# Performance work log

Hardware: AMD Instinct MI355X
Metric: run time of the kernel (lower is better)

## Reference

```python
import jax, jax.numpy as jnp
import numpy as np

B, S, D = 4, 512, 2048      # batch, seq, hidden
DFF = 5632                   # SwiGLU intermediate
E, TOPK, R = 8, 2, 16        # experts, top-k, lora rank
SCALE = 32.0 / 16.0          # lora alpha / r


def setup_inputs() -> dict:
    key = jax.random.key(0)
    ks = jax.random.split(key, 18)
    rn = lambda k, shape, s=0.02: (jax.random.normal(k, shape, dtype=jnp.float32) * s)
    return {
        "data": jax.random.normal(ks[0], (B, S, D), dtype=jnp.float32),
        # shared base SwiGLU MLP (gate/up/down projections)
        "W1": rn(ks[1], (DFF, D)),
        "W3": rn(ks[2], (DFF, D)),
        "W2": rn(ks[3], (D, DFF)),
        # MixLoRA MoE adapter: router gate + per-expert LoRA on w1/w3/w2
        "gate_W": rn(ks[4], (E, D)),
        "A1": rn(ks[5], (E, R, D)), "B1": rn(ks[6], (E, DFF, R)),
        "A3": rn(ks[7], (E, R, D)), "B3": rn(ks[8], (E, DFF, R)),
        "A2": rn(ks[9], (E, R, DFF)), "B2": rn(ks[10], (E, D, R)),
        # plain LoRA adapter (second batch segment, _lora_forward path)
        "la1": rn(ks[11], (R, D)), "lb1": rn(ks[12], (DFF, R)),
        "la3": rn(ks[13], (R, D)), "lb3": rn(ks[14], (DFF, R)),
        "la2": rn(ks[15], (R, DFF)), "lb2": rn(ks[16], (D, R)),
    }


def reference(data, W1, W3, W2, gate_W, A1, B1, A3, B3, A2, B2,
              la1, lb1, la3, lb3, la2, lb2):
    half = B // 2

    # ---- segment 0: MixLoRA MoE adapter ----
    x = data[:half].reshape(-1, D)                      # [N, D] tokens
    N = x.shape[0]
    logits = x @ gate_W.T                               # [N, E] router logits
    probs = jax.nn.softmax(logits, axis=-1)
    topw, topi = jax.lax.top_k(probs, TOPK)
    topw = topw / jnp.sum(topw, axis=-1, keepdims=True)
    # dense routing weights (zero for non-selected experts)
    wd = jnp.zeros((N, E), x.dtype).at[jnp.arange(N)[:, None], topi].set(topw)

    bg = x @ W1.T                                       # [N, DFF] base gate proj
    bu = x @ W3.T                                       # [N, DFF] base up proj
    dg = jnp.einsum('enr,efr->enf', jnp.einsum('nd,erd->enr', x, A1), B1)
    du = jnp.einsum('enr,efr->enf', jnp.einsum('nd,erd->enr', x, A3), B3)
    h = jax.nn.silu(bg[None] + SCALE * dg) * (bu[None] + SCALE * du)  # [E,N,DFF]
    oe = jnp.einsum('enf,df->end', h, W2) \
        + SCALE * jnp.einsum('enr,edr->end', jnp.einsum('enf,erf->enr', h, A2), B2)
    moe_out = jnp.einsum('ne,end->nd', wd, oe).reshape(half, S, D)

    # ---- segment 1: plain LoRA adapter (_lora_forward) ----
    x2 = data[half:]                                    # [half, S, D]
    g2 = jax.nn.silu(x2 @ W1.T + SCALE * ((x2 @ la1.T) @ lb1.T))
    u2 = x2 @ W3.T + SCALE * ((x2 @ la3.T) @ lb3.T)
    h2 = g2 * u2
    out2 = h2 @ W2.T + SCALE * ((h2 @ la2.T) @ lb2.T)

    # index_copy over contiguous per-segment ranges == concat along dim 0
    final = jnp.concatenate([moe_out, out2], axis=0)    # [B, S, D]
    return final, logits
```

## Files before the change

### kernel.cpp

```cpp
#include <hip/hip_runtime.h>
#include <hip/hip_bf16.h>

#define DEVI __device__ __forceinline__

typedef __attribute__((ext_vector_type(8))) short short8;
typedef __attribute__((ext_vector_type(4))) float f32x4;

constexpr int D    = 2048;
constexpr int DFF  = 5632;
constexpr int NTOK = 2048;
constexpr int NMOE = 1024;
constexpr float KSCALE = 2.0f;

constexpr int NW      = 11776;
constexpr int COL_A1  = 11264;
constexpr int COL_A3  = 11392;
constexpr int COL_LA1 = 11520;
constexpr int COL_LA3 = 11536;

DEVI float bf2f(unsigned short u) { return __uint_as_float(((unsigned)u) << 16); }
DEVI unsigned short f2bf(float f) {
  unsigned u = __float_as_uint(f);
  u += 0x7FFFu + ((u >> 16) & 1u);
  return (unsigned short)(u >> 16);
}
DEVI float silu(float x) { return x / (1.f + __expf(-x)); }

struct CastSegs {
  const float* src[14];
  unsigned short* dst[14];
  int blk_end[14];
};

__global__ __launch_bounds__(256) void cast_segs_kernel(CastSegs cs) {
  int b = blockIdx.x;
  int s = 0;
  #pragma unroll
  for (int i = 0; i < 14; ++i) if (b >= cs.blk_end[i]) s = i + 1;
  int bstart = (s == 0) ? 0 : cs.blk_end[s - 1];
  size_t idx = ((size_t)(b - bstart) * 256 + threadIdx.x) * 4;
  float4 v = *(const float4*)(cs.src[s] + idx);
  ushort4 o;
  o.x = f2bf(v.x); o.y = f2bf(v.y); o.z = f2bf(v.z); o.w = f2bf(v.w);
  *(ushort4*)(cs.dst[s] + idx) = o;
}

__global__ __launch_bounds__(256) void transpose_ra_kernel(const float* __restrict__ A2,
                                                           const float* __restrict__ la2,
                                                           unsigned short* __restrict__ A2tb,
                                                           unsigned short* __restrict__ la2tb) {
  int f = blockIdx.x * 256 + threadIdx.x;
  int e = blockIdx.y;
  const float* src = (e < 8) ? (A2 + (size_t)e * 16 * DFF) : la2;
  unsigned short* dst = (e < 8) ? (A2tb + (size_t)e * DFF * 16) : la2tb;
  unsigned short tmp[16];
  #pragma unroll
  for (int r = 0; r < 16; ++r) tmp[r] = f2bf(src[(size_t)r * DFF + f]);
  #pragma unroll
  for (int r = 0; r < 16; ++r) dst[(size_t)f * 16 + r] = tmp[r];
}

__global__ __launch_bounds__(256) void gate_kernel(const float* __restrict__ x,
                                                   const float* __restrict__ gW,
                                                   float* __restrict__ logits_out,
                                                   int* __restrict__ gidx,
                                                   float* __restrict__ gwt) {
  int t = blockIdx.x * 4 + (threadIdx.x >> 6);
  int lane = threadIdx.x & 63;
  const float* xr = x + (size_t)t * D;
  float acc[8];
  #pragma unroll
  for (int e = 0; e < 8; ++e) acc[e] = 0.f;
  for (int k = lane; k < D; k += 64) {
    float xv = xr[k];
    #pragma unroll
    for (int e = 0; e < 8; ++e) acc[e] = fmaf(xv, gW[e * D + k], acc[e]);
  }
  #pragma unroll
  for (int e = 0; e < 8; ++e) {
    float v = acc[e];
    #pragma unroll
    for (int s = 32; s > 0; s >>= 1) v += __shfl_xor(v, s);
    acc[e] = v;
  }
  if (lane == 0) {
    #pragma unroll
    for (int e = 0; e < 8; ++e) logits_out[(size_t)t * 8 + e] = acc[e];
    int i1 = 0;
    #pragma unroll
    for (int e = 1; e < 8; ++e) if (acc[e] > acc[i1]) i1 = e;
    int i2 = (i1 == 0) ? 1 : 0;
    #pragma unroll
    for (int e = 0; e < 8; ++e) if (e != i1 && acc[e] > acc[i2]) i2 = e;
    float w1 = 1.f / (1.f + expf(acc[i2] - acc[i1]));
    gidx[t * 2] = i1; gidx[t * 2 + 1] = i2;
    gwt[t * 2] = w1;  gwt[t * 2 + 1] = 1.f - w1;
  }
}

typedef const void __attribute__((address_space(1)))* gp1_t;
typedef void __attribute__((address_space(3)))* lp3_t;
DEVI void gload_lds16(const void* g, void* l) {
  __builtin_amdgcn_global_load_lds((gp1_t)g, (lp3_t)l, 16, 0, 0);
}
#define S_BARRIER() asm volatile("s_barrier" ::: "memory")
#define LGKM0() do { asm volatile("s_waitcnt lgkmcnt(0)" ::: "memory"); \
                     __builtin_amdgcn_sched_barrier(0); } while (0)

template <int N> DEVI void vmcnt_() {
  static_assert(N == 0 || N == 4 || N == 8, "enumerate literals");
  if constexpr (N == 0)  asm volatile("s_waitcnt vmcnt(0)" ::: "memory");
  if constexpr (N == 4)  asm volatile("s_waitcnt vmcnt(4)" ::: "memory");
  if constexpr (N == 8)  asm volatile("s_waitcnt vmcnt(8)" ::: "memory");
}

template <int BM, int BN, int WM, int WN, int MINW, int EPI>
__global__ __launch_bounds__(WM * WN * 64, MINW) void gemm8p(
    const unsigned short* __restrict__ A,
    const unsigned short* __restrict__ B,
    int K,
    float* __restrict__ Cf,
    unsigned short* __restrict__ Cb,
    const float* __restrict__ addv,
    int ldc, int nbx) {
  constexpr int THREADS = WM * WN * 64;
  constexpr int RW = BM / WM;
  constexpr int CW = BN / WN;
  constexpr int FM = RW / 16, FN = CW / 16;
  constexpr int FM2 = FM / 2;
  constexpr int ATILE = BM * 128;
  constexpr int BTILE = BN * 128;
  constexpr int SLOT = ATILE + BTILE;
  constexpr int APARTS = BM * 8 / THREADS;
  constexpr int BPARTS = BN * 8 / THREADS;
  constexpr int LOADS = APARTS + BPARTS;

  __shared__ __align__(16) char smem[2 * SLOT];

  const int tid = threadIdx.x;
  const int wave = tid >> 6, lane = tid & 63;
  const int wm = wave / WN, wn = wave % WN;
  const int r15 = lane & 15, g = lane >> 4;

  const int nwg = (int)gridDim.x;
  const int bid = (int)blockIdx.x;
  const int wgid = (bid & 7) * (nwg >> 3) + (bid >> 3);
  const int bx = wgid % nbx, by = wgid / nbx;

  const unsigned short* Ablk = A + (size_t)by * BM * K;
  const unsigned short* Bblk = B + (size_t)bx * BN * K;

  int sgoA[APARTS], sgoB[BPARTS];
  #pragma unroll
  for (int j = 0; j < APARTS; ++j) {
    int tt = j * THREADS + tid;
    int row = tt >> 3;
    sgoA[j] = row * K + (((tt & 7) ^ (row & 7)) << 3);
  }
  #pragma unroll
  for (int j = 0; j < BPARTS; ++j) {
    int tt = j * THREADS + tid;
    int row = tt >> 3;
    sgoB[j] = row * K + (((tt & 7) ^ (row & 7)) << 3);
  }
  auto stage = [&](int slot, int k0) {
    char* s = smem + slot * SLOT;
    #pragma unroll
    for (int j = 0; j < APARTS; ++j)
      gload_lds16((const char*)Ablk + ((size_t)(sgoA[j] + k0) << 1),
                  s + j * (THREADS * 16) + wave * 1024);
    #pragma unroll
    for (int j = 0; j < BPARTS; ++j)
      gload_lds16((const char*)Bblk + ((size_t)(sgoB[j] + k0) << 1),
                  s + ATILE + j * (THREADS * 16) + wave * 1024);
  };

  const int arow0 = (wm * RW + r15) * 128;
  const int brow0 = (wn * CW + r15) * 128;
  const int s0 = ((g ^ (r15 & 7)) << 4);
  const int s1 = (((4 + g) ^ (r15 & 7)) << 4);

  f32x4 acc[FM][FN];
  #pragma unroll
  for (int m = 0; m < FM; ++m)
    #pragma unroll
    for (int n = 0; n < FN; ++n)
      #pragma unroll
      for (int j = 0; j < 4; ++j) acc[m][n][j] = 0.f;

  const int NT = K >> 6;

  stage(0, 0);

  for (int t = 0; t < NT; ++t) {
    const int cur = t & 1;
    if (t + 1 < NT) {
      stage(cur ^ 1, (t + 1) << 6);
      vmcnt_<LOADS>();
    } else {
      vmcnt_<0>();
    }
    S_BARRIER();

    const char* sA = smem + cur * SLOT;
    const char* sB = sA + ATILE;

    short8 bq[FN][2];
    #pragma unroll
    for (int n = 0; n < FN; ++n) {
      bq[n][0] = *(const short8*)(sB + brow0 + n * 16 * 128 + s0);
      bq[n][1] = *(const short8*)(sB + brow0 + n * 16 * 128 + s1);
    }
    short8 af0[FM2][2];
    #pragma unroll
    for (int i = 0; i < FM2; ++i) {
      int ro = arow0 + i * 16 * 128;
      af0[i][0] = *(const short8*)(sA + ro + s0);
      af0[i][1] = *(const short8*)(sA + ro + s1);
    }
    S_BARRIER();
    LGKM0();
    __builtin_amdgcn_s_setprio(1);
    #pragma unroll
    for (int i = 0; i < FM2; ++i)
      #pragma unroll
      for (int n = 0; n < FN; ++n)
        #pragma unroll
        for (int kk = 0; kk < 2; ++kk)
          acc[i][n] = __builtin_amdgcn_mfma_f32_16x16x32_bf16(
              af0[i][kk], bq[n][kk], acc[i][n], 0, 0, 0);
    __builtin_amdgcn_s_setprio(0);

    short8 af1[FM2][2];
    #pragma unroll
    for (int i = 0; i < FM2; ++i) {
      int ro = arow0 + (FM2 + i) * 16 * 128;
      af1[i][0] = *(const short8*)(sA + ro + s0);
      af1[i][1] = *(const short8*)(sA + ro + s1);
    }
    S_BARRIER();
    LGKM0();
    __builtin_amdgcn_s_setprio(1);
    #pragma unroll
    for (int i = 0; i < FM2; ++i)
      #pragma unroll
      for (int n = 0; n < FN; ++n)
        #pragma unroll
        for (int kk = 0; kk < 2; ++kk)
          acc[FM2 + i][n] = __builtin_amdgcn_mfma_f32_16x16x32_bf16(
              af1[i][kk], bq[n][kk], acc[FM2 + i][n], 0, 0, 0);
    __builtin_amdgcn_s_setprio(0);

    S_BARRIER();
  }

  const int row0 = by * BM + wm * RW + (g << 2);
  const int col0 = bx * BN + wn * CW + r15;
  #pragma unroll
  for (int m = 0; m < FM; ++m) {
    #pragma unroll
    for (int n = 0; n < FN; ++n) {
      int col = col0 + n * 16;
      #pragma unroll
      for (int j = 0; j < 4; ++j) {
        int row = row0 + m * 16 + j;
        size_t off = (size_t)row * ldc + col;
        float v = acc[m][n][j];
        if (EPI == 1) Cb[off] = f2bf(v);
        else          Cf[off] = v + addv[off];
      }
    }
  }
}

DEVI float dot16bf(const float* a, const unsigned short* w) {
  short8 w0 = *(const short8*)w;
  short8 w1 = *(const short8*)(w + 8);
  float s = 0.f;
  #pragma unroll
  for (int i = 0; i < 8; ++i) s = fmaf(a[i],     bf2f((unsigned short)w0[i]), s);
  #pragma unroll
  for (int i = 0; i < 8; ++i) s = fmaf(a[8 + i], bf2f((unsigned short)w1[i]), s);
  return s;
}

__global__ __launch_bounds__(256) void h_kernel(
    const unsigned short* __restrict__ GU,
    const unsigned short* __restrict__ B1b,
    const unsigned short* __restrict__ B3b,
    const unsigned short* __restrict__ A2tb,
    const unsigned short* __restrict__ lb1b,
    const unsigned short* __restrict__ lb3b,
    const unsigned short* __restrict__ la2tb,
    const int* __restrict__ gidx, const float* __restrict__ gwt,
    unsigned short* __restrict__ Hb,
    float* __restrict__ qw) {
  const int t = blockIdx.x;
  const int tid = threadIdx.x;
  const unsigned short* gu = GU + (size_t)t * NW;
  unsigned short* hrow = Hb + (size_t)t * DFF;
  float qacc[32];
  #pragma unroll
  for (int r = 0; r < 32; ++r) qacc[r] = 0.f;
  float w1 = 0.f, w2 = 0.f;

  if (t < NMOE) {
    const int e1 = gidx[t * 2], e2 = gidx[t * 2 + 1];
    w1 = gwt[t * 2]; w2 = gwt[t * 2 + 1];
    float xa1a[16], xa1b[16], xa3a[16], xa3b[16];
    #pragma unroll
    for (int r = 0; r < 16; ++r) {
      xa1a[r] = bf2f(gu[COL_A1 + e1 * 16 + r]);
      xa1b[r] = bf2f(gu[COL_A1 + e2 * 16 + r]);
      xa3a[r] = bf2f(gu[COL_A3 + e1 * 16 + r]);
      xa3b[r] = bf2f(gu[COL_A3 + e2 * 16 + r]);
    }
    const unsigned short* B1e1 = B1b + (size_t)e1 * DFF * 16;
    const unsigned short* B1e2 = B1b + (size_t)e2 * DFF * 16;
    const unsigned short* B3e1 = B3b + (size_t)e1 * DFF * 16;
    const unsigned short* B3e2 = B3b + (size_t)e2 * DFF * 16;
    const unsigned short* A2e1 = A2tb + (size_t)e1 * DFF * 16;
    const unsigned short* A2e2 = A2tb + (size_t)e2 * DFF * 16;
    for (int i = 0; i < 22; ++i) {
      int f = tid + i * 256;
      float bg = bf2f(gu[f]), bu = bf2f(gu[DFF + f]);
      float dg1 = dot16bf(xa1a, B1e1 + f * 16);
      float du1 = dot16bf(xa3a, B3e1 + f * 16);
      float dg2 = dot16bf(xa1b, B1e2 + f * 16);
      float du2 = dot16bf(xa3b, B3e2 + f * 16);
      float h1 = silu(bg + KSCALE * dg1) * (bu + KSCALE * du1);
      float h2 = silu(bg + KSCALE * dg2) * (bu + KSCALE * du2);
      hrow[f] = f2bf(w1 * h1 + w2 * h2);
      short8 a0 = *(const short8*)(A2e1 + f * 16);
      short8 a1 = *(const short8*)(A2e1 + f * 16 + 8);
      short8 b0 = *(const short8*)(A2e2 + f * 16);
      short8 b1 = *(const short8*)(A2e2 + f * 16 + 8);
      #pragma unroll
      for (int r = 0; r < 8; ++r) {
        qacc[r]      = fmaf(h1, bf2f((unsigned short)a0[r]), qacc[r]);
        qacc[8 + r]  = fmaf(h1, bf2f((unsigned short)a1[r]), qacc[8 + r]);
        qacc[16 + r] = fmaf(h2, bf2f((unsigned short)b0[r]), qacc[16 + r]);
        qacc[24 + r] = fmaf(h2, bf2f((unsigned short)b1[r]), qacc[24 + r]);
      }
    }
  } else {
    float s1[16], s3[16];
    #pragma unroll
    for (int r = 0; r < 16; ++r) {
      s1[r] = bf2f(gu[COL_LA1 + r]);
      s3[r] = bf2f(gu[COL_LA3 + r]);
    }
    for (int i = 0; i < 22; ++i) {
      int f = tid + i * 256;
      float bg = bf2f(gu[f]), bu = bf2f(gu[DFF + f]);
      float dg = dot16bf(s1, lb1b + f * 16);
      float du = dot16bf(s3, lb3b + f * 16);
      float h = silu(bg + KSCALE * dg) * (bu + KSCALE * du);
      hrow[f] = f2bf(h);
      short8 a0 = *(const short8*)(la2tb + f * 16);
      short8 a1 = *(const short8*)(la2tb + f * 16 + 8);
      #pragma unroll
      for (int r = 0; r < 8; ++r) {
        qacc[r]     = fmaf(h, bf2f((unsigned short)a0[r]), qacc[r]);
        qacc[8 + r] = fmaf(h, bf2f((unsigned short)a1[r]), qacc[8 + r]);
      }
    }
  }

  #pragma unroll
  for (int r = 0; r < 32; ++r) {
    float v = qacc[r];
    #pragma unroll
    for (int s = 32; s > 0; s >>= 1) v += __shfl_xor(v, s);
    qacc[r] = v;
  }
  __shared__ float red[4][32];
  const int wave = tid >> 6, lane = tid & 63;
  if (lane == 0) {
    #pragma unroll
    for (int r = 0; r < 32; ++r) red[wave][r] = qacc[r];
  }
  __syncthreads();
  if (tid < 32) {
    float v = red[0][tid] + red[1][tid] + red[2][tid] + red[3][tid];
    float sc = (t < NMOE) ? ((tid < 16) ? (KSCALE * w1) : (KSCALE * w2)) : KSCALE;
    qw[(size_t)t * 32 + tid] = v * sc;
  }
}

__global__ __launch_bounds__(256) void ylora_kernel(const float* __restrict__ qw,
                                                    const unsigned short* __restrict__ B2b,
                                                    const unsigned short* __restrict__ lb2b,
                                                    const int* __restrict__ gidx,
                                                    float* __restrict__ ylora) {
  const int t = blockIdx.x;
  const int tid = threadIdx.x;
  const float* qr = qw + (size_t)t * 32;
  float q1[16], q2[16];
  #pragma unroll
  for (int r = 0; r < 16; ++r) { q1[r] = qr[r]; q2[r] = qr[16 + r]; }
  if (t < NMOE) {
    const unsigned short* p1 = B2b + (size_t)gidx[t * 2] * D * 16;
    const unsigned short* p2 = B2b + (size_t)gidx[t * 2 + 1] * D * 16;
    #pragma unroll
    for (int i = 0; i < 8; ++i) {
      int d = tid + i * 256;
      ylora[(size_t)t * D + d] = dot16bf(q1, p1 + d * 16) + dot16bf(q2, p2 + d * 16);
    }
  } else {
    #pragma unroll
    for (int i = 0; i < 8; ++i) {
      int d = tid + i * 256;
      ylora[(size_t)t * D + d] = dot16bf(q1, lb2b + d * 16);
    }
  }
}

extern "C" void kernel_launch(void* const* d_in, const int* in_sizes, int n_in,
                              void* d_out, int out_size, void* d_ws, size_t ws_size,
                              hipStream_t stream) {
  (void)in_sizes; (void)n_in; (void)out_size; (void)ws_size;
  const float* data = (const float*)d_in[0];
  const float* W1   = (const float*)d_in[1];
  const float* W3   = (const float*)d_in[2];
  const float* W2   = (const float*)d_in[3];
  const float* gW   = (const float*)d_in[4];
  const float* A1   = (const float*)d_in[5];
  const float* B1   = (const float*)d_in[6];
  const float* A3   = (const float*)d_in[7];
  const float* B3   = (const float*)d_in[8];
  const float* A2   = (const float*)d_in[9];
  const float* B2   = (const float*)d_in[10];
  const float* la1  = (const float*)d_in[11];
  const float* lb1  = (const float*)d_in[12];
  const float* la3  = (const float*)d_in[13];
  const float* lb3  = (const float*)d_in[14];
  const float* la2  = (const float*)d_in[15];
  const float* lb2  = (const float*)d_in[16];

  char* w = (char*)d_ws;
  size_t off = 0;
  auto alloc = [&](size_t bytes) -> char* {
    char* p = w + off;
    off += (bytes + 255) & ~(size_t)255;
    return p;
  };
  unsigned short* xb    = (unsigned short*)alloc((size_t)NTOK * D * 2);
  unsigned short* W13b  = (unsigned short*)alloc((size_t)NW * D * 2);
  unsigned short* W2b   = (unsigned short*)alloc((size_t)D * DFF * 2);
  unsigned short* B1b   = (unsigned short*)alloc((size_t)8 * DFF * 16 * 2);
  unsigned short* B3b   = (unsigned short*)alloc((size_t)8 * DFF * 16 * 2);
  unsigned short* A2tb  = (unsigned short*)alloc((size_t)8 * DFF * 16 * 2);
  unsigned short* la2tb = (unsigned short*)alloc((size_t)DFF * 16 * 2);
  unsigned short* lb1b  = (unsigned short*)alloc((size_t)DFF * 16 * 2);
  unsigned short* lb3b  = (unsigned short*)alloc((size_t)DFF * 16 * 2);
  unsigned short* lb2b  = (unsigned short*)alloc((size_t)D * 16 * 2);
  unsigned short* B2b   = (unsigned short*)alloc((size_t)8 * D * 16 * 2);
  int*   gidx = (int*)alloc((size_t)NMOE * 2 * 4);
  float* gwt  = (float*)alloc((size_t)NMOE * 2 * 4);
  unsigned short* GU    = (unsigned short*)alloc((size_t)NTOK * NW * 2);

  unsigned short* Hb = W13b;
  float* ylora = (float*)((char*)W13b + (size_t)NTOK * DFF * 2);
  float* qw    = (float*)xb;

  CastSegs cs;
  const float* srcs[14] = {data, W1, W3, W2, A1, A3, la1, la3, B1, B3, lb1, lb3, lb2, B2};
  unsigned short* dsts[14] = {
      xb, W13b, W13b + (size_t)DFF * D, W2b,
      W13b + (size_t)COL_A1 * D, W13b + (size_t)COL_A3 * D,
      W13b + (size_t)COL_LA1 * D, W13b + (size_t)COL_LA3 * D,
      B1b, B3b, lb1b, lb3b, lb2b, B2b};
  int ns[14] = {NTOK * D, DFF * D, DFF * D, DFF * D, 128 * D, 128 * D, 16 * D, 16 * D,
                8 * DFF * 16, 8 * DFF * 16, DFF * 16, DFF * 16, D * 16, 8 * D * 16};
  int total_blocks = 0;
  for (int i = 0; i < 14; ++i) {
    cs.src[i] = srcs[i];
    cs.dst[i] = dsts[i];
    total_blocks += ns[i] / 1024;
    cs.blk_end[i] = total_blocks;
  }
  cast_segs_kernel<<<total_blocks, 256, 0, stream>>>(cs);
  transpose_ra_kernel<<<dim3(DFF / 256, 9), 256, 0, stream>>>(A2, la2, A2tb, la2tb);
  hipMemsetAsync(W13b + (size_t)11552 * D, 0, (size_t)(NW - 11552) * D * 2, stream);

  gate_kernel<<<NMOE / 4, 256, 0, stream>>>(data, gW,
      (float*)d_out + (size_t)NTOK * D, gidx, gwt);

  gemm8p<256, 256, 2, 4, 2, 1><<<(NTOK / 256) * (NW / 256), 512, 0, stream>>>(
      xb, W13b, D, (float*)nullptr, GU, (const float*)nullptr, NW, NW / 256);

  h_kernel<<<NTOK, 256, 0, stream>>>(GU, B1b, B3b, A2tb, lb1b, lb3b, la2tb,
                                     gidx, gwt, Hb, qw);

  ylora_kernel<<<NTOK, 256, 0, stream>>>(qw, B2b, lb2b, gidx, ylora);

  gemm8p<128, 128, 2, 4, 4, 2><<<(NTOK / 128) * (D / 128), 512, 0, stream>>>(
      Hb, W2b, DFF, (float*)d_out, (unsigned short*)nullptr, ylora, D, D / 128);
}
```

Measured before the change: 367.1 us.

## Split B-tile staging across compute phases, retile GEMMs and trim column padding

The GEMM kernel now assumes a fixed 64x64 tile per wave. It issues only the A-tile prefetch at the top of each k-step and spreads the two halves of the B-tile prefetch across the two MFMA phases, so global-to-LDS traffic overlaps compute more evenly and the vmcnt wait is shallower. The gate/up GEMM moves from 256x256 to 256x128 tiles with a 4x2 wave grid. Its padded weight width drops from 11776 to 11648 columns, which removes wasted zero-column work and gives more workgroups. The down-projection GEMM now uses 256-thread 128x128 blocks with different occupancy bounds. The risks are lower reuse per tile in the first GEMM and changed occupancy and latency hiding in both GEMMs.

```diff
diff --git a/kernel.cpp b/kernel.cpp
--- a/kernel.cpp
+++ b/kernel.cpp
@@ -12,7 +12,7 @@
 constexpr int NMOE = 1024;
 constexpr float KSCALE = 2.0f;
 
-constexpr int NW      = 11776;
+constexpr int NW      = 11648;
 constexpr int COL_A1  = 11264;
 constexpr int COL_A3  = 11392;
 constexpr int COL_LA1 = 11520;
@@ -108,14 +108,13 @@
                      __builtin_amdgcn_sched_barrier(0); } while (0)
 
 template <int N> DEVI void vmcnt_() {
-  static_assert(N == 0 || N == 4 || N == 8, "enumerate literals");
+  static_assert(N == 0 || N == 4, "enumerate literals");
   if constexpr (N == 0)  asm volatile("s_waitcnt vmcnt(0)" ::: "memory");
   if constexpr (N == 4)  asm volatile("s_waitcnt vmcnt(4)" ::: "memory");
-  if constexpr (N == 8)  asm volatile("s_waitcnt vmcnt(8)" ::: "memory");
 }
 
 template <int BM, int BN, int WM, int WN, int MINW, int EPI>
-__global__ __launch_bounds__(WM * WN * 64, MINW) void gemm8p(
+__global__ __launch_bounds__(WM * WN * 64, MINW) void gemmP(
     const unsigned short* __restrict__ A,
     const unsigned short* __restrict__ B,
     int K,
@@ -126,14 +125,13 @@
   constexpr int THREADS = WM * WN * 64;
   constexpr int RW = BM / WM;
   constexpr int CW = BN / WN;
-  constexpr int FM = RW / 16, FN = CW / 16;
-  constexpr int FM2 = FM / 2;
+  static_assert(RW == 64 && CW == 64, "template assumes 64x64 per-wave tile");
   constexpr int ATILE = BM * 128;
   constexpr int BTILE = BN * 128;
   constexpr int SLOT = ATILE + BTILE;
   constexpr int APARTS = BM * 8 / THREADS;
   constexpr int BPARTS = BN * 8 / THREADS;
-  constexpr int LOADS = APARTS + BPARTS;
+  constexpr int BH = BPARTS / 2;
 
   __shared__ __align__(16) char smem[2 * SLOT];
 
@@ -163,16 +161,19 @@
     int row = tt >> 3;
     sgoB[j] = row * K + (((tt & 7) ^ (row & 7)) << 3);
   }
-  auto stage = [&](int slot, int k0) {
-    char* s = smem + slot * SLOT;
+  auto stageA = [&](int p, int k0) {
+    char* s = smem + p * SLOT;
     #pragma unroll
     for (int j = 0; j < APARTS; ++j)
       gload_lds16((const char*)Ablk + ((size_t)(sgoA[j] + k0) << 1),
                   s + j * (THREADS * 16) + wave * 1024);
-    #pragma unroll
-    for (int j = 0; j < BPARTS; ++j)
-      gload_lds16((const char*)Bblk + ((size_t)(sgoB[j] + k0) << 1),
-                  s + ATILE + j * (THREADS * 16) + wave * 1024);
+  };
+  auto stageBh = [&](int p, int k0, int h) {
+    char* s = smem + p * SLOT + ATILE;
+    #pragma unroll
+    for (int j = 0; j < BH; ++j)
+      gload_lds16((const char*)Bblk + ((size_t)(sgoB[h * BH + j] + k0) << 1),
+                  s + (h * BH + j) * (THREADS * 16) + wave * 1024);
   };
 
   const int arow0 = (wm * RW + r15) * 128;
@@ -180,75 +181,78 @@
   const int s0 = ((g ^ (r15 & 7)) << 4);
   const int s1 = (((4 + g) ^ (r15 & 7)) << 4);
 
-  f32x4 acc[FM][FN];
-  #pragma unroll
-  for (int m = 0; m < FM; ++m)
-    #pragma unroll
-    for (int n = 0; n < FN; ++n)
+  f32x4 acc[4][4];
+  #pragma unroll
+  for (int m = 0; m < 4; ++m)
+    #pragma unroll
+    for (int n = 0; n < 4; ++n)
       #pragma unroll
       for (int j = 0; j < 4; ++j) acc[m][n][j] = 0.f;
 
   const int NT = K >> 6;
 
-  stage(0, 0);
+  stageA(0, 0);
+  stageBh(0, 0, 0);
+  stageBh(0, 0, 1);
 
   for (int t = 0; t < NT; ++t) {
-    const int cur = t & 1;
-    if (t + 1 < NT) {
-      stage(cur ^ 1, (t + 1) << 6);
-      vmcnt_<LOADS>();
+    const int p = t & 1;
+    const bool hn = (t + 1) < NT;
+    const int k0n = (t + 1) << 6;
+    if (hn) {
+      stageA(p ^ 1, k0n);
+      vmcnt_<4>();
     } else {
       vmcnt_<0>();
     }
     S_BARRIER();
 
-    const char* sA = smem + cur * SLOT;
+    const char* sA = smem + p * SLOT;
     const char* sB = sA + ATILE;
 
-    short8 bq[FN][2];
-    #pragma unroll
-    for (int n = 0; n < FN; ++n) {
-      bq[n][0] = *(const short8*)(sB + brow0 + n * 16 * 128 + s0);
-      bq[n][1] = *(const short8*)(sB + brow0 + n * 16 * 128 + s1);
-    }
-    short8 af0[FM2][2];
-    #pragma unroll
-    for (int i = 0; i < FM2; ++i) {
-      int ro = arow0 + i * 16 * 128;
-      af0[i][0] = *(const short8*)(sA + ro + s0);
-      af0[i][1] = *(const short8*)(sA + ro + s1);
-    }
+    short8 bq[4][2], af[2][2];
+    #pragma unroll
+    for (int n = 0; n < 4; ++n) {
+      bq[n][0] = *(const short8*)(sB + brow0 + n * 2048 + s0);
+      bq[n][1] = *(const short8*)(sB + brow0 + n * 2048 + s1);
+    }
+    #pragma unroll
+    for (int i = 0; i < 2; ++i) {
+      af[i][0] = *(const short8*)(sA + arow0 + i * 2048 + s0);
+      af[i][1] = *(const short8*)(sA + arow0 + i * 2048 + s1);
+    }
+    if (hn) stageBh(p ^ 1, k0n, 0);
     S_BARRIER();
     LGKM0();
     __builtin_amdgcn_s_setprio(1);
     #pragma unroll
-    for (int i = 0; i < FM2; ++i)
+    for (int i = 0; i < 2; ++i)
       #pragma unroll
-      for (int n = 0; n < FN; ++n)
+      for (int n = 0; n < 4; ++n)
         #pragma unroll
         for (int kk = 0; kk < 2; ++kk)
           acc[i][n] = __builtin_amdgcn_mfma_f32_16x16x32_bf16(
-              af0[i][kk], bq[n][kk], acc[i][n], 0, 0, 0);
+              af[i][kk], bq[n][kk], acc[i][n], 0, 0, 0);
     __builtin_amdgcn_s_setprio(0);
 
-    short8 af1[FM2][2];
-    #pragma unroll
-    for (int i = 0; i < FM2; ++i) {
-      int ro = arow0 + (FM2 + i) * 16 * 128;
-      af1[i][0] = *(const short8*)(sA + ro + s0);
-      af1[i][1] = *(const short8*)(sA + ro + s1);
-    }
+    short8 ag[2][2];
+    #pragma unroll
+    for (int i = 0; i < 2; ++i) {
+      ag[i][0] = *(const short8*)(sA + arow0 + (2 + i) * 2048 + s0);
+      ag[i][1] = *(const short8*)(sA + arow0 + (2 + i) * 2048 + s1);
+    }
+    if (hn) stageBh(p ^ 1, k0n, 1);
     S_BARRIER();
     LGKM0();
     __builtin_amdgcn_s_setprio(1);
     #pragma unroll
-    for (int i = 0; i < FM2; ++i)
+    for (int i = 0; i < 2; ++i)
       #pragma unroll
-      for (int n = 0; n < FN; ++n)
+      for (int n = 0; n < 4; ++n)
         #pragma unroll
         for (int kk = 0; kk < 2; ++kk)
-          acc[FM2 + i][n] = __builtin_amdgcn_mfma_f32_16x16x32_bf16(
-              af1[i][kk], bq[n][kk], acc[FM2 + i][n], 0, 0, 0);
+          acc[2 + i][n] = __builtin_amdgcn_mfma_f32_16x16x32_bf16(
+              ag[i][kk], bq[n][kk], acc[2 + i][n], 0, 0, 0);
     __builtin_amdgcn_s_setprio(0);
 
     S_BARRIER();
@@ -257,9 +261,9 @@
   const int row0 = by * BM + wm * RW + (g << 2);
   const int col0 = bx * BN + wn * CW + r15;
   #pragma unroll
-  for (int m = 0; m < FM; ++m) {
-    #pragma unroll
-    for (int n = 0; n < FN; ++n) {
+  for (int m = 0; m < 4; ++m) {
+    #pragma unroll
+    for (int n = 0; n < 4; ++n) {
       int col = col0 + n * 16;
       #pragma unroll
       for (int j = 0; j < 4; ++j) {
@@ -487,14 +491,14 @@
   gate_kernel<<<NMOE / 4, 256, 0, stream>>>(data, gW,
       (float*)d_out + (size_t)NTOK * D, gidx, gwt);
 
-  gemm8p<256, 256, 2, 4, 2, 1><<<(NTOK / 256) * (NW / 256), 512, 0, stream>>>(
-      xb, W13b, D, (float*)nullptr, GU, (const float*)nullptr, NW, NW / 256);
+  gemmP<256, 128, 4, 2, 2, 1><<<(NTOK / 256) * (NW / 128), 512, 0, stream>>>(
+      xb, W13b, D, (float*)nullptr, GU, (const float*)nullptr, NW, NW / 128);
 
   h_kernel<<<NTOK, 256, 0, stream>>>(GU, B1b, B3b, A2tb, lb1b, lb3b, la2tb,
                                      gidx, gwt, Hb, qw);
 
   ylora_kernel<<<NTOK, 256, 0, stream>>>(qw, B2b, lb2b, gidx, ylora);
 
-  gemm8p<128, 128, 2, 4, 4, 2><<<(NTOK / 128) * (D / 128), 512, 0, stream>>>(
+  gemmP<128, 128, 2, 2, 2, 2><<<(NTOK / 128) * (D / 128), 256, 0, stream>>>(
       Hb, W2b, DFF, (float*)d_out, (unsigned short*)nullptr, ylora, D, D / 128);
 }
```

After: 358.1 us. -2.4%, faster.
